# Performance work log

Hardware: AMD Instinct MI355X
Metric: run time of the kernel (lower is better)

## Reference

```python
import jax, jax.numpy as jnp
import numpy as np

OBS_LEN = 20
K = 20          # number of latent samples (leading dim of pred_lstm_hidden)
B = 4096        # batch
C = 2           # n_coordinates
H = 128         # z_dim + s_dim
MH = 64         # mapping hidden dim


def hardsigmoid(x):
    return jnp.clip(x / 6.0 + 0.5, 0.0, 1.0)


def hardtanh(x):
    return jnp.clip(x, -1.0, 1.0)


def setup_inputs() -> dict:
    key = jax.random.key(0)
    ks = jax.random.split(key, 12)
    std = 0.1  # _initialize_weights: normal(0, 0.1), biases zero
    return {
        "obs_traj_rel": jax.random.normal(ks[0], (OBS_LEN, B, C), jnp.float32),
        "pred_lstm_hidden": jax.random.normal(ks[1], (K, B, H), jnp.float32),
        # mapping MLP: Linear(H, MH) + LeakyReLU, Linear(MH, H)
        "Wm1": std * jax.random.normal(ks[2], (MH, H), jnp.float32),
        "bm1": jnp.zeros((MH,), jnp.float32),
        "Wm2": std * jax.random.normal(ks[3], (H, MH), jnp.float32),
        "bm2": jnp.zeros((H,), jnp.float32),
        # custom LSTMCell params
        "W_ih": std * jax.random.normal(ks[4], (4 * H, C), jnp.float32),
        "W_hh": std * jax.random.normal(ks[5], (4 * H, H), jnp.float32),
        "b_ih": jnp.zeros((4 * H,), jnp.float32),
        "b_hh": jnp.zeros((4 * H,), jnp.float32),
        # pred_hidden2pos: Linear(H, C)
        "W_out": std * jax.random.normal(ks[6], (C, H), jnp.float32),
        "b_out": jnp.zeros((C,), jnp.float32),
    }


def reference(obs_traj_rel, pred_lstm_hidden, Wm1, bm1, Wm2, bm2,
              W_ih, W_hh, b_ih, b_hh, W_out, b_out):
    # mapping MLP over last dim: [K, B, H]
    h = jax.nn.leaky_relu(jnp.einsum('kbh,mh->kbm', pred_lstm_hidden, Wm1) + bm1)
    h = jnp.einsum('kbm,hm->kbh', h, Wm2) + bm2
    c = jnp.zeros_like(h)

    # step i uses obs_traj_rel[max(i-1, 0)]
    idx = np.concatenate([[0], np.arange(OBS_LEN - 1)])
    inputs_seq = obs_traj_rel[idx, :, :C]  # [T, B, C]

    def step(carry, x_t):
        h, c = carry  # each [K, B, H]
        # input term is identical across the K samples -> compute once, broadcast
        gi = x_t @ W_ih.T + b_ih                      # [B, 4H]
        gh = jnp.einsum('kbh,gh->kbg', h, W_hh) + b_hh  # [K, B, 4H]
        gates = gi[None] + gh
        i_g, f_g, g_g, o_g = jnp.split(gates, 4, axis=-1)
        c_new = hardsigmoid(f_g) * c + hardsigmoid(i_g) * hardtanh(g_g)
        h_new = hardsigmoid(o_g) * hardtanh(c_new)
        out = jnp.einsum('kbh,ch->kbc', h_new, W_out) + b_out  # [K, B, C]
        return (h_new, c_new), out

    _, outs = jax.lax.scan(step, (h, c), inputs_seq)
    return outs  # [obs_len, K, B, C]
```

## Files before the change

### kernel.cpp

```cpp
#include <hip/hip_runtime.h>

#define NT 20
#define BT 4096
#define HD 128
#define RT 81920
#define RB 64

typedef _Float16 half8 __attribute__((ext_vector_type(8)));
typedef _Float16 half2v __attribute__((ext_vector_type(2)));
typedef float f32x4 __attribute__((ext_vector_type(4)));
typedef float f32x2 __attribute__((ext_vector_type(2)));
typedef unsigned u32x4 __attribute__((ext_vector_type(4)));

#if defined(__has_builtin)
#  if __has_builtin(__builtin_amdgcn_fdot2)
#    define HAVE_FDOT2 1
#  endif
#endif

__device__ __forceinline__ float hsig(float x) {
  return fminf(fmaxf(x * 0.16666667f + 0.5f, 0.0f), 1.0f);
}
__device__ __forceinline__ float htanh(float x) {
  return fminf(fmaxf(x, -1.0f), 1.0f);
}

__device__ __forceinline__ float dot2(half2v a, half2v b, float c) {
#ifdef HAVE_FDOT2
  return __builtin_amdgcn_fdot2(a, b, c, false);
#else
  return fmaf((float)a[0], (float)b[0], fmaf((float)a[1], (float)b[1], c));
#endif
}

__device__ __forceinline__ half8 ldcvt8(const float* __restrict__ p) {
  f32x4 a = *(const f32x4*)p;
  f32x4 b = *(const f32x4*)(p + 4);
  half8 r;
  r[0] = (_Float16)a[0]; r[1] = (_Float16)a[1];
  r[2] = (_Float16)a[2]; r[3] = (_Float16)a[3];
  r[4] = (_Float16)b[0]; r[5] = (_Float16)b[1];
  r[6] = (_Float16)b[2]; r[7] = (_Float16)b[3];
  return r;
}

__device__ __forceinline__ void lds_barrier() {
  __builtin_amdgcn_sched_barrier(0);
  asm volatile("s_waitcnt lgkmcnt(0)" ::: "memory");
  __builtin_amdgcn_s_barrier();
  __builtin_amdgcn_sched_barrier(0);
}

__global__ __launch_bounds__(512, 2) void decoder_kernel(
    const float* __restrict__ obs, const float* __restrict__ pred,
    const float* __restrict__ Wm1, const float* __restrict__ bm1,
    const float* __restrict__ Wm2, const float* __restrict__ bm2,
    const float* __restrict__ W_ih, const float* __restrict__ W_hh,
    const float* __restrict__ b_ih, const float* __restrict__ b_hh,
    const float* __restrict__ W_out, const float* __restrict__ b_out,
    float* __restrict__ outp)
{
  __shared__ __align__(16) char lds[71168];
  const int tid = threadIdx.x;
  const int w   = tid >> 6;
  const int l   = tid & 63;
  const int l15 = l & 15;
  const int lg  = l >> 4;
  const int wm  = w & 3;
  const int wc  = w >> 2;
  const int r0  = blockIdx.x * RB;
  const int b0  = r0 & (BT - 1);

  char* const buf0 = lds;
  char* const h1l  = lds + 16384;
  char* const cstl = lds + 32768;
  char* const obsl = lds + 65536;
  char* const wol  = lds + 70656;

  const f32x4 fzero = {0.f, 0.f, 0.f, 0.f};

  const int rdmask = (l15 & 7) << 4;
  const int arow  = l15 * 256;
  const int base0 = (16 * lg) ^ rdmask;
  const int wcol2 = 32 * w + 2 * l15;
  const int cb    = tid * 16;

  if (tid < 256) ((_Float16*)wol)[tid] = (_Float16)W_out[tid];
  for (int i = tid; i < NT * RB; i += 512) {
    int t = i >> 6, row = i & 63;
    int tp = (t > 0) ? t - 1 : 0;
    f32x2 xv = *(const f32x2*)(obs + ((size_t)tp * BT + b0 + row) * 2);
    half2v hp; hp[0] = (_Float16)xv[0]; hp[1] = (_Float16)xv[1];
    *(unsigned*)(obsl + (size_t)i * 4) = __builtin_bit_cast(unsigned, hp);
  }
#pragma unroll
  for (int mm = 0; mm < 4; ++mm)
    *(f32x4*)(cstl + mm * 8192 + cb) = fzero;

  {
    half8 a1[4], b1[2][4];
#pragma unroll
    for (int kt = 0; kt < 4; ++kt)
      a1[kt] = ldcvt8(pred + (size_t)(r0 + 16 * wm + l15) * HD + kt * 32 + lg * 8);
#pragma unroll
    for (int j = 0; j < 2; ++j)
#pragma unroll
      for (int kt = 0; kt < 4; ++kt)
        b1[j][kt] = ldcvt8(Wm1 + (l15 + 16 * (2 * wc + j)) * HD + kt * 32 + lg * 8);
    f32x4 acc1[2] = {fzero, fzero};
#pragma unroll
    for (int kt = 0; kt < 4; ++kt)
#pragma unroll
      for (int j = 0; j < 2; ++j)
        acc1[j] = __builtin_amdgcn_mfma_f32_16x16x32_f16(a1[kt], b1[j][kt], acc1[j], 0, 0, 0);
#pragma unroll
    for (int j = 0; j < 2; ++j) {
      int c = l15 + 16 * (2 * wc + j);
      float bb = bm1[c];
#pragma unroll
      for (int reg = 0; reg < 4; ++reg) {
        int row = 16 * wm + 4 * lg + reg;
        float v = acc1[j][reg] + bb;
        v = v >= 0.f ? v : 0.01f * v;
        *(_Float16*)(h1l + row * 128 + ((2 * c) ^ ((row & 7) << 4))) = (_Float16)v;
      }
    }
  }
  __syncthreads();
  {
    half8 a2[2], b2[4][2];
#pragma unroll
    for (int kt = 0; kt < 2; ++kt)
      a2[kt] = *(const half8*)(h1l + (16 * wm + l15) * 128 + ((64 * kt + 16 * lg) ^ rdmask));
#pragma unroll
    for (int j = 0; j < 4; ++j)
#pragma unroll
      for (int kt = 0; kt < 2; ++kt)
        b2[j][kt] = ldcvt8(Wm2 + (l15 + 16 * (4 * wc + j)) * 64 + kt * 32 + lg * 8);
    f32x4 acc2[4] = {fzero, fzero, fzero, fzero};
#pragma unroll
    for (int kt = 0; kt < 2; ++kt)
#pragma unroll
      for (int j = 0; j < 4; ++j)
        acc2[j] = __builtin_amdgcn_mfma_f32_16x16x32_f16(a2[kt], b2[j][kt], acc2[j], 0, 0, 0);
#pragma unroll
    for (int j = 0; j < 4; ++j) {
      int c = l15 + 16 * (4 * wc + j);
      float bb = bm2[c];
#pragma unroll
      for (int reg = 0; reg < 4; ++reg) {
        int row = 16 * wm + 4 * lg + reg;
        float v = acc2[j][reg] + bb;
        *(_Float16*)(buf0 + row * 256 + ((2 * c) ^ ((row & 7) << 4))) = (_Float16)v;
      }
    }
  }

  half8 bW[4][4];
  unsigned awp[4], abp[4];
#pragma unroll
  for (int n = 0; n < 4; ++n) {
    int g = 128 * n + 16 * w + l15;
#pragma unroll
    for (int kt = 0; kt < 4; ++kt)
      bW[n][kt] = ldcvt8(W_hh + (size_t)g * HD + kt * 32 + lg * 8);
    half2v t2;
    t2[0] = (_Float16)W_ih[g * 2 + 0];
    t2[1] = (_Float16)W_ih[g * 2 + 1];
    awp[n] = __builtin_bit_cast(unsigned, t2);
    half2v t3;
    t3[0] = (_Float16)(b_ih[g] + b_hh[g]);
    t3[1] = (_Float16)0.0f;
    abp[n] = __builtin_bit_cast(unsigned, t3);
  }
  const float bo = wc ? b_out[1] : b_out[0];

  __syncthreads();

  for (int t = 0; t < NT; ++t) {
    char* const brd = lds + ((t & 1) << 14);
    char* const bwr = lds + (((t & 1) ^ 1) << 14);

#pragma unroll
    for (int j = 0; j < 4; ++j) {
      const int mm = (wm + wc + 1 + j) & 3;
      f32x4 cc = *(const f32x4*)(cstl + mm * 8192 + cb);

      f32x4 acc[4] = {fzero, fzero, fzero, fzero};
      const bool doFold = (j == 3 - wc) && (t > 0);
      float p = 0.f;

      __builtin_amdgcn_s_setprio(1);
#pragma unroll
      for (int kt = 0; kt < 5; ++kt) {
        half8 a;
        if (kt < 4) {
          a = *(const half8*)(brd + mm * 4096 + arow + ((64 * kt) ^ base0));
          if (doFold) {
            const half8 wf = *(const half8*)(wol + wc * 256 + kt * 64 + lg * 16);
#pragma unroll
            for (int pp = 0; pp < 4; ++pp) {
              half2v ha; ha[0] = a[2 * pp]; ha[1] = a[2 * pp + 1];
              half2v wa; wa[0] = wf[2 * pp]; wa[1] = wf[2 * pp + 1];
              p = dot2(ha, wa, p);
            }
          }
        } else {
          unsigned xv = *(const unsigned*)(obsl + ((t << 6) + (mm << 4) + l15) * 4);
          unsigned u0 = (lg == 0) ? xv : 0u;
          unsigned u1 = (lg == 0) ? 0x00003C00u : 0u;
          u32x4 xu = {u0, u1, 0u, 0u};
          a = __builtin_bit_cast(half8, xu);
        }
#pragma unroll
        for (int n = 0; n < 4; ++n) {
          half8 bfrag;
          if (kt < 4) {
            bfrag = bW[n][kt];
          } else {
            unsigned v0 = (lg == 0) ? awp[n] : 0u;
            unsigned v1 = (lg == 0) ? abp[n] : 0u;
            u32x4 bu = {v0, v1, 0u, 0u};
            bfrag = __builtin_bit_cast(half8, bu);
          }
          acc[n] = __builtin_amdgcn_mfma_f32_16x16x32_f16(a, bfrag, acc[n], 0, 0, 0);
        }
      }
      __builtin_amdgcn_s_setprio(0);

      if (doFold) {
        p += __shfl_xor(p, 16, 64); p += __shfl_xor(p, 32, 64);
        if (l < 16)
          outp[(size_t)(t - 1) * (RT * 2) + (size_t)(r0 + 16 * wm + l) * 2 + wc] = p + bo;
      }

      f32x4 cn4;
#pragma unroll
      for (int reg = 0; reg < 4; ++reg) {
        float cn = hsig(acc[1][reg]) * cc[reg] + hsig(acc[0][reg]) * htanh(acc[2][reg]);
        cn4[reg] = cn;
        float hn = hsig(acc[3][reg]) * htanh(cn);
        int rr = 4 * lg + reg;
        int wb = rr * 256 + (wcol2 ^ ((rr & 7) << 4));
        *(_Float16*)(bwr + mm * 4096 + wb) = (_Float16)hn;
      }
      *(f32x4*)(cstl + mm * 8192 + cb) = cn4;
    }
    lds_barrier();
  }

  {
    float p = 0.f;
#pragma unroll
    for (int kt = 0; kt < 4; ++kt) {
      half8 a = *(const half8*)(buf0 + wm * 4096 + arow + ((64 * kt) ^ base0));
      const half8 wf = *(const half8*)(wol + wc * 256 + kt * 64 + lg * 16);
#pragma unroll
      for (int pp = 0; pp < 4; ++pp) {
        half2v ha; ha[0] = a[2 * pp]; ha[1] = a[2 * pp + 1];
        half2v wa; wa[0] = wf[2 * pp]; wa[1] = wf[2 * pp + 1];
        p = dot2(ha, wa, p);
      }
    }
    p += __shfl_xor(p, 16, 64); p += __shfl_xor(p, 32, 64);
    if (l < 16)
      outp[(size_t)19 * (RT * 2) + (size_t)(r0 + 16 * wm + l) * 2 + wc] = p + bo;
  }
}

extern "C" void kernel_launch(void* const* d_in, const int* in_sizes, int n_in,
                              void* d_out, int out_size, void* d_ws, size_t ws_size,
                              hipStream_t stream) {
  const float* obs   = (const float*)d_in[0];
  const float* pred  = (const float*)d_in[1];
  const float* Wm1   = (const float*)d_in[2];
  const float* bm1   = (const float*)d_in[3];
  const float* Wm2   = (const float*)d_in[4];
  const float* bm2   = (const float*)d_in[5];
  const float* W_ih  = (const float*)d_in[6];
  const float* W_hh  = (const float*)d_in[7];
  const float* b_ih  = (const float*)d_in[8];
  const float* b_hh  = (const float*)d_in[9];
  const float* W_out = (const float*)d_in[10];
  const float* b_out = (const float*)d_in[11];

  decoder_kernel<<<RT / RB, 512, 0, stream>>>(
      obs, pred, Wm1, bm1, Wm2, bm2, W_ih, W_hh, b_ih, b_hh, W_out, b_out,
      (float*)d_out);
}
```

Before: 322.0 us.

## Software-pipeline gate MFMAs with previous tile's elementwise and fold hardsigmoid scale

The recurrent step loop now double-buffers the gate accumulators, so the elementwise LSTM update of the previous row tile runs while the MFMAs of the current tile are issued. All A fragments are loaded up front. The 1/6 scale and +0.5 offset of hardsigmoid are folded into the f16 W_hh, W_ih and bias fragments, so the activation becomes a plain clamp. The output projection is moved to the last tile of each step using the fragments already in registers. This adds register pressure from the second accumulator set and the preloaded fragments, and scaling the weights to f16 slightly changes rounding.

```diff
diff --git a/kernel.cpp b/kernel.cpp
--- a/kernel.cpp
+++ b/kernel.cpp
@@ -18,8 +18,8 @@
 #  endif
 #endif
 
-__device__ __forceinline__ float hsig(float x) {
-  return fminf(fmaxf(x * 0.16666667f + 0.5f, 0.0f), 1.0f);
+__device__ __forceinline__ float clamp01(float x) {
+  return fminf(fmaxf(x, 0.0f), 1.0f);
 }
 __device__ __forceinline__ float htanh(float x) {
   return fminf(fmaxf(x, -1.0f), 1.0f);
@@ -33,15 +33,18 @@
 #endif
 }
 
-__device__ __forceinline__ half8 ldcvt8(const float* __restrict__ p) {
+__device__ __forceinline__ half8 ldcvt8s(const float* __restrict__ p, float s) {
   f32x4 a = *(const f32x4*)p;
   f32x4 b = *(const f32x4*)(p + 4);
   half8 r;
-  r[0] = (_Float16)a[0]; r[1] = (_Float16)a[1];
-  r[2] = (_Float16)a[2]; r[3] = (_Float16)a[3];
-  r[4] = (_Float16)b[0]; r[5] = (_Float16)b[1];
-  r[6] = (_Float16)b[2]; r[7] = (_Float16)b[3];
+  r[0] = (_Float16)(a[0] * s); r[1] = (_Float16)(a[1] * s);
+  r[2] = (_Float16)(a[2] * s); r[3] = (_Float16)(a[3] * s);
+  r[4] = (_Float16)(b[0] * s); r[5] = (_Float16)(b[1] * s);
+  r[6] = (_Float16)(b[2] * s); r[7] = (_Float16)(b[3] * s);
   return r;
+}
+__device__ __forceinline__ half8 ldcvt8(const float* __restrict__ p) {
+  return ldcvt8s(p, 1.0f);
 }
 
 __device__ __forceinline__ void lds_barrier() {
@@ -78,6 +81,7 @@
   char* const wol  = lds + 70656;
 
   const f32x4 fzero = {0.f, 0.f, 0.f, 0.f};
+  const float SCL = 1.0f / 6.0f;
 
   const int rdmask = (l15 & 7) << 4;
   const int arow  = l15 * 256;
@@ -160,16 +164,18 @@
   unsigned awp[4], abp[4];
 #pragma unroll
   for (int n = 0; n < 4; ++n) {
+    const float s = (n == 2) ? 1.0f : SCL;
     int g = 128 * n + 16 * w + l15;
 #pragma unroll
     for (int kt = 0; kt < 4; ++kt)
-      bW[n][kt] = ldcvt8(W_hh + (size_t)g * HD + kt * 32 + lg * 8);
+      bW[n][kt] = ldcvt8s(W_hh + (size_t)g * HD + kt * 32 + lg * 8, s);
     half2v t2;
-    t2[0] = (_Float16)W_ih[g * 2 + 0];
-    t2[1] = (_Float16)W_ih[g * 2 + 1];
+    t2[0] = (_Float16)(W_ih[g * 2 + 0] * s);
+    t2[1] = (_Float16)(W_ih[g * 2 + 1] * s);
     awp[n] = __builtin_bit_cast(unsigned, t2);
+    float bs = b_ih[g] + b_hh[g];
     half2v t3;
-    t3[0] = (_Float16)(b_ih[g] + b_hh[g]);
+    t3[0] = (_Float16)((n == 2) ? bs : bs * SCL + 0.5f);
     t3[1] = (_Float16)0.0f;
     abp[n] = __builtin_bit_cast(unsigned, t3);
   }
@@ -181,37 +187,52 @@
     char* const brd = lds + ((t & 1) << 14);
     char* const bwr = lds + (((t & 1) ^ 1) << 14);
 
+    f32x4 acc[2][4];
+    f32x4 ccp = fzero;
+    int   mmp = 0;
+
 #pragma unroll
     for (int j = 0; j < 4; ++j) {
-      const int mm = (wm + wc + 1 + j) & 3;
+      const int mm = (wm + 1 + j) & 3;
+      const int b  = j & 1;
+
       f32x4 cc = *(const f32x4*)(cstl + mm * 8192 + cb);
 
-      f32x4 acc[4] = {fzero, fzero, fzero, fzero};
-      const bool doFold = (j == 3 - wc) && (t > 0);
-      float p = 0.f;
-
+      half8 af[5];
+#pragma unroll
+      for (int kt = 0; kt < 4; ++kt)
+        af[kt] = *(const half8*)(brd + mm * 4096 + arow + ((64 * kt) ^ base0));
+      {
+        unsigned xv = *(const unsigned*)(obsl + ((t << 6) + (mm << 4) + l15) * 4);
+        unsigned u0 = (lg == 0) ? xv : 0u;
+        unsigned u1 = (lg == 0) ? 0x00003C00u : 0u;
+        u32x4 xu = {u0, u1, 0u, 0u};
+        af[4] = __builtin_bit_cast(half8, xu);
+      }
+
+      if (j > 0) {
+        f32x4 cn4;
+#pragma unroll
+        for (int reg = 0; reg < 4; ++reg) {
+          float i_ = clamp01(acc[b ^ 1][0][reg]);
+          float f_ = clamp01(acc[b ^ 1][1][reg]);
+          float g_ = htanh(acc[b ^ 1][2][reg]);
+          float o_ = clamp01(acc[b ^ 1][3][reg]);
+          float cn = fmaf(f_, ccp[reg], i_ * g_);
+          cn4[reg] = cn;
+          float hn = o_ * htanh(cn);
+          int rr = 4 * lg + reg;
+          int wb = rr * 256 + (wcol2 ^ ((rr & 7) << 4));
+          *(_Float16*)(bwr + mmp * 4096 + wb) = (_Float16)hn;
+        }
+        *(f32x4*)(cstl + mmp * 8192 + cb) = cn4;
+      }
+
+#pragma unroll
+      for (int n = 0; n < 4; ++n) acc[b][n] = fzero;
       __builtin_amdgcn_s_setprio(1);
 #pragma unroll
       for (int kt = 0; kt < 5; ++kt) {
-        half8 a;
-        if (kt < 4) {
-          a = *(const half8*)(brd + mm * 4096 + arow + ((64 * kt) ^ base0));
-          if (doFold) {
-            const half8 wf = *(const half8*)(wol + wc * 256 + kt * 64 + lg * 16);
-#pragma unroll
-            for (int pp = 0; pp < 4; ++pp) {
-              half2v ha; ha[0] = a[2 * pp]; ha[1] = a[2 * pp + 1];
-              half2v wa; wa[0] = wf[2 * pp]; wa[1] = wf[2 * pp + 1];
-              p = dot2(ha, wa, p);
-            }
-          }
-        } else {
-          unsigned xv = *(const unsigned*)(obsl + ((t << 6) + (mm << 4) + l15) * 4);
-          unsigned u0 = (lg == 0) ? xv : 0u;
-          unsigned u1 = (lg == 0) ? 0x00003C00u : 0u;
-          u32x4 xu = {u0, u1, 0u, 0u};
-          a = __builtin_bit_cast(half8, xu);
-        }
 #pragma unroll
         for (int n = 0; n < 4; ++n) {
           half8 bfrag;
@@ -223,28 +244,49 @@
             u32x4 bu = {v0, v1, 0u, 0u};
             bfrag = __builtin_bit_cast(half8, bu);
           }
-          acc[n] = __builtin_amdgcn_mfma_f32_16x16x32_f16(a, bfrag, acc[n], 0, 0, 0);
+          acc[b][n] = __builtin_amdgcn_mfma_f32_16x16x32_f16(af[kt], bfrag, acc[b][n], 0, 0, 0);
         }
       }
       __builtin_amdgcn_s_setprio(0);
 
-      if (doFold) {
+      if (j == 3 && t > 0) {
+        float p = 0.f;
+#pragma unroll
+        for (int kt = 0; kt < 4; ++kt) {
+          const half8 a = af[kt];
+          const half8 wf = *(const half8*)(wol + wc * 256 + kt * 64 + lg * 16);
+#pragma unroll
+          for (int pp = 0; pp < 4; ++pp) {
+            half2v ha; ha[0] = a[2 * pp]; ha[1] = a[2 * pp + 1];
+            half2v wa; wa[0] = wf[2 * pp]; wa[1] = wf[2 * pp + 1];
+            p = dot2(ha, wa, p);
+          }
+        }
         p += __shfl_xor(p, 16, 64); p += __shfl_xor(p, 32, 64);
         if (l < 16)
           outp[(size_t)(t - 1) * (RT * 2) + (size_t)(r0 + 16 * wm + l) * 2 + wc] = p + bo;
       }
 
+      ccp = cc;
+      mmp = mm;
+    }
+
+    {
       f32x4 cn4;
 #pragma unroll
       for (int reg = 0; reg < 4; ++reg) {
-        float cn = hsig(acc[1][reg]) * cc[reg] + hsig(acc[0][reg]) * htanh(acc[2][reg]);
+        float i_ = clamp01(acc[1][0][reg]);
+        float f_ = clamp01(acc[1][1][reg]);
+        float g_ = htanh(acc[1][2][reg]);
+        float o_ = clamp01(acc[1][3][reg]);
+        float cn = fmaf(f_, ccp[reg], i_ * g_);
         cn4[reg] = cn;
-        float hn = hsig(acc[3][reg]) * htanh(cn);
+        float hn = o_ * htanh(cn);
         int rr = 4 * lg + reg;
         int wb = rr * 256 + (wcol2 ^ ((rr & 7) << 4));
-        *(_Float16*)(bwr + mm * 4096 + wb) = (_Float16)hn;
-      }
-      *(f32x4*)(cstl + mm * 8192 + cb) = cn4;
+        *(_Float16*)(bwr + mmp * 4096 + wb) = (_Float16)hn;
+      }
+      *(f32x4*)(cstl + mmp * 8192 + cb) = cn4;
     }
     lds_barrier();
   }
```

After: 322.8 us. About the same (+0.2%).
